# Kernel optimization log

Measured on AMD Instinct MI355X. Metric: run time of the kernel, lower is better.

Reference implementation:

```python
import jax, jax.numpy as jnp
import numpy as np

ALPHA = 4.0          # spikingjelly default surrogate.Sigmoid(alpha=4.0)
V_TH = 1.0           # IFNode default v_threshold
BN_EPS = 1e-5

@jax.custom_vjp
def spike(x):
    # heaviside forward
    return (x >= 0.0).astype(x.dtype)

def _spike_fwd(x):
    return spike(x), x

def _spike_bwd(x, g):
    s = jax.nn.sigmoid(ALPHA * x)
    return (g * ALPHA * s * (1.0 - s),)

spike.defvjp(_spike_fwd, _spike_bwd)

def if_node(x_seq):
    """Multi-step IF neuron: integrate, threshold, hard reset (v_reset=0),
    detach_reset=True. x_seq: [T, ...] -> spikes [T, ...]."""
    def step(v, xt):
        v = v + xt
        s = spike(v - V_TH)
        v = v * (1.0 - jax.lax.stop_gradient(s))  # detached hard reset to 0
        return v, s
    _, s_seq = jax.lax.scan(step, jnp.zeros_like(x_seq[0]), x_seq)
    return s_seq

def bn1d(x, gamma, beta):
    """Training-mode BatchNorm1d over flattened (T*B) batch dim. x: [T,B,F]."""
    m = x.mean(axis=(0, 1))
    v = x.var(axis=(0, 1))  # biased variance, matches torch normalization
    return (x - m) * jax.lax.rsqrt(v + BN_EPS) * gamma + beta

def setup_inputs() -> dict:
    key = jax.random.key(0)
    ks = jax.random.split(key, 12)
    T, B, C, H, W = 8, 64, 2, 128, 128
    F0, D, NC = C * H * W, 2048, 1000
    x = jax.random.uniform(ks[0], (T, B, C, H, W), dtype=jnp.float32)
    def kaiming(k, out_f, in_f):
        # kaiming_normal_ mode='fan_out', relu gain: std = sqrt(2/out_f)
        return jax.random.normal(k, (out_f, in_f), dtype=jnp.float32) * np.sqrt(2.0 / out_f)
    def bias(k, out_f, in_f):
        bound = 1.0 / np.sqrt(in_f)
        return jax.random.uniform(k, (out_f,), dtype=jnp.float32, minval=-bound, maxval=bound)
    inp = {"x": x}
    dims = [(D, F0), (D, D), (D, D)]
    for i, (o, f) in enumerate(dims):
        inp[f"W{i}"] = kaiming(ks[1 + i], o, f)
        inp[f"b{i}"] = bias(ks[4 + i], o, f)
        inp[f"g{i}"] = jnp.ones((o,), jnp.float32)
        inp[f"be{i}"] = jnp.zeros((o,), jnp.float32)
    inp["Wout"] = kaiming(ks[7], NC, D)
    inp["bout"] = bias(ks[8], NC, D)
    return inp

def reference(x, W0, b0, g0, be0, W1, b1, g1, be1, W2, b2, g2, be2, Wout, bout):
    T, B = x.shape[0], x.shape[1]
    h = x.reshape(T, B, -1)           # [T,B,32768]
    h = if_node(h)                    # sn0
    for Wl, bl, gl, bel in ((W0, b0, g0, be0), (W1, b1, g1, be1), (W2, b2, g2, be2)):
        h = jnp.einsum('tbi,oi->tbo', h, Wl) + bl
        h = bn1d(h, gl, bel)
        h = if_node(h)
    out = jnp.einsum('tbi,oi->tbo', h, Wout) + bout  # [T,B,1000]
    return out.mean(axis=0)           # [B,1000]
```

## Files before the change

### kernel.cpp

```cpp
#include <hip/hip_runtime.h>


#define T_STEPS 8
#define BATCH 64
#define F0 32768
#define DIM 2048
#define NROWS 512
#define NC 1000

typedef __attribute__((ext_vector_type(8))) short short8;
typedef __attribute__((ext_vector_type(4))) float f32x4;

__device__ __forceinline__ unsigned short bf16_rne(float f) {
    unsigned int u = __float_as_uint(f);
    u += 0x7FFFu + ((u >> 16) & 1u);
    return (unsigned short)(u >> 16);
}

#define BM 128
#define BN 128
#define BK 32

__global__ __launch_bounds__(256, 3) void gemm_splitk(
    const unsigned short* __restrict__ A, const float* __restrict__ W,
    float* __restrict__ part, int M, int N, int K, int Kpart, int Wrows)
{
    __shared__ unsigned short As[2][BM * BK];
    __shared__ unsigned short HL[2][BN * 64];

    const int gx = gridDim.x, gy = gridDim.y;
    const int nwg = gx * gy * gridDim.z;
    const int lid = blockIdx.x + gx * (blockIdx.y + gy * blockIdx.z);
    const int cpx = nwg >> 3;
    const int nid = (lid & 7) * cpx + (lid >> 3);
    const int bx  = nid % gx;
    const int by  = (nid / gx) % gy;
    const int kz  = nid / (gx * gy);

    const int tid  = threadIdx.x;
    const int lane = tid & 63;
    const int w    = tid >> 6;
    const int bm   = bx * BM;
    const int bn   = by * BN;
    const int ksteps = Kpart / BK;
    const int wm = (w >> 1) * 64;
    const int wn = (w & 1) * 64;
    const int kbase = kz * Kpart;

    const int a_sl  = ((lane & 3) ^ ((lane >> 3) & 3)) << 4;
    const int a_row = lane >> 2;

    const int wn_row = tid >> 3;
    const int wc4    = tid & 7;
    const int r7     = wn_row & 7;
    const int hi_off = (((wc4 >> 1) ^ r7) << 4) + (wc4 & 1) * 8;
    const int lo_off = ((((wc4 >> 1) + 4) ^ r7) << 4) + (wc4 & 1) * 8;

    const int l15 = lane & 15;
    const int a_ph = (((lane >> 4) ^ ((l15 >> 1) & 3)) << 4);
    const int h_ph = (((lane >> 4) ^ (lane & 7)) << 4);
    const int l_ph = ((((lane >> 4) + 4) ^ (lane & 7)) << 4);

    f32x4 acc[4][4] = {};
    float4 wv[4];

    auto issue_loads = [&](int buf, int kt) {
        const int k0 = kbase + kt * BK;
#pragma unroll
        for (int i = 0; i < 4; ++i) {
            const int rg = min(bn + wn_row + 32 * i, Wrows - 1);
            wv[i] = *(const float4*)&W[(size_t)rg * K + k0 + wc4 * 4];
        }
#pragma unroll
        for (int c = 0; c < 2; ++c) {
            const int row = w * 32 + c * 16 + a_row;
            const char* src = (const char*)A + ((size_t)(bm + row) * K + k0) * 2 + a_sl;
            __builtin_amdgcn_global_load_lds(
                (const __attribute__((address_space(1))) void*)src,
                (__attribute__((address_space(3))) void*)&As[buf][(w * 32 + c * 16) * BK],
                16, 0, 0);
        }
    };
    auto convert_write = [&](int buf) {
#pragma unroll
        for (int i = 0; i < 4; ++i) {
            const float vf[4] = {wv[i].x, wv[i].y, wv[i].z, wv[i].w};
            unsigned short h[4], l[4];
#pragma unroll
            for (int e = 0; e < 4; ++e) {
                h[e] = bf16_rne(vf[e]);
                l[e] = bf16_rne(vf[e] - __uint_as_float((unsigned int)h[e] << 16));
            }
            char* base = (char*)&HL[buf][0] + (wn_row + 32 * i) * 128;
            *(ushort4*)(base + hi_off) = make_ushort4(h[0], h[1], h[2], h[3]);
            *(ushort4*)(base + lo_off) = make_ushort4(l[0], l[1], l[2], l[3]);
        }
    };

    issue_loads(0, 0);
    convert_write(0);
    __syncthreads();

    int cur = 0;
    for (int kt = 0; kt < ksteps; ++kt) {
        const bool last = (kt + 1 == ksteps);
        if (!last) issue_loads(cur ^ 1, kt + 1);

        short8 a[4];
#pragma unroll
        for (int mi = 0; mi < 4; ++mi)
            a[mi] = *(const short8*)((const char*)&As[cur][0] + (wm + mi * 16 + l15) * 64 + a_ph);
#pragma unroll
        for (int ni = 0; ni < 4; ++ni) {
            const char* rp = (const char*)&HL[cur][0] + (wn + ni * 16 + l15) * 128;
            const short8 bh = *(const short8*)(rp + h_ph);
            const short8 bl = *(const short8*)(rp + l_ph);
#pragma unroll
            for (int mi = 0; mi < 4; ++mi) {
                acc[mi][ni] = __builtin_amdgcn_mfma_f32_16x16x32_bf16(a[mi], bh, acc[mi][ni], 0, 0, 0);
                acc[mi][ni] = __builtin_amdgcn_mfma_f32_16x16x32_bf16(a[mi], bl, acc[mi][ni], 0, 0, 0);
            }
        }
        if (!last) convert_write(cur ^ 1);
        __syncthreads();
        cur ^= 1;
    }

    const size_t zoff = (size_t)kz * M * N;
#pragma unroll
    for (int mi = 0; mi < 4; ++mi) {
        const int gr0 = bm + wm + mi * 16 + (lane >> 4) * 4;
#pragma unroll
        for (int ni = 0; ni < 4; ++ni) {
            const int gc = bn + wn + ni * 16 + (lane & 15);
            if (gc < N) {
#pragma unroll
                for (int e = 0; e < 4; ++e) {
                    const int gr = gr0 + e;
                    if (gr < M) part[zoff + (size_t)gr * N + gc] = acc[mi][ni][e];
                }
            }
        }
    }
}

__global__ __launch_bounds__(256) void reduce_bias(
    const float* __restrict__ part, const float* __restrict__ bias,
    float* __restrict__ out, int KS, int MN, int N)
{
    const int i4 = blockIdx.x * 256 + threadIdx.x;
    if (i4 * 4 >= MN) return;
    float4 s = make_float4(0.f, 0.f, 0.f, 0.f);
    for (int z = 0; z < KS; ++z) {
        const float4 p = *(const float4*)&part[(size_t)z * MN + i4 * 4];
        s.x += p.x; s.y += p.y; s.z += p.z; s.w += p.w;
    }
    const int col = (i4 * 4) % N;
    const float4 b = *(const float4*)&bias[col];
    s.x += b.x; s.y += b.y; s.z += b.z; s.w += b.w;
    *(float4*)&out[(size_t)i4 * 4] = s;
}

__global__ __launch_bounds__(256) void if0_kernel(
    const float* __restrict__ x, unsigned short* __restrict__ s)
{
    const size_t id4 = ((size_t)blockIdx.x * 256 + threadIdx.x) * 4;
    float v0 = 0.f, v1 = 0.f, v2 = 0.f, v3 = 0.f;
#pragma unroll
    for (int t = 0; t < T_STEPS; ++t) {
        const size_t idx = (size_t)t * (BATCH * (size_t)F0) + id4;
        const float4 xv = *(const float4*)&x[idx];
        ushort4 o;
        v0 += xv.x; if (v0 >= 1.f) { o.x = 0x3F80; v0 = 0.f; } else o.x = 0;
        v1 += xv.y; if (v1 >= 1.f) { o.y = 0x3F80; v1 = 0.f; } else o.y = 0;
        v2 += xv.z; if (v2 >= 1.f) { o.z = 0x3F80; v2 = 0.f; } else o.z = 0;
        v3 += xv.w; if (v3 >= 1.f) { o.w = 0x3F80; v3 = 0.f; } else o.w = 0;
        *(ushort4*)&s[idx] = o;
    }
}

__global__ __launch_bounds__(256) void bn_stats_if(
    const float* __restrict__ z, const float* __restrict__ g,
    const float* __restrict__ be, unsigned short* __restrict__ s)
{
    __shared__ float ssum[4][64], ssq[4][64];
    __shared__ float ssc[64], ssh[64];
    const int l = threadIdx.x & 63;
    const int q = threadIdx.x >> 6;
    const int f = blockIdx.x * 64 + l;
    float sum = 0.f, sq = 0.f;
    for (int r = q; r < NROWS; r += 4) {
        const float v = z[(size_t)r * DIM + f];
        sum += v; sq += v * v;
    }
    ssum[q][l] = sum; ssq[q][l] = sq;
    __syncthreads();
    if (threadIdx.x < 64) {
        float ts = 0.f, tq = 0.f;
#pragma unroll
        for (int i = 0; i < 4; ++i) { ts += ssum[i][l]; tq += ssq[i][l]; }
        const float mean = ts * (1.0f / NROWS);
        const float var  = tq * (1.0f / NROWS) - mean * mean;
        const float inv  = rsqrtf(var + 1e-5f);
        const float sc   = g[f] * inv;
        ssc[l] = sc;
        ssh[l] = be[f] - mean * sc;
    }
    __syncthreads();
    const float sc = ssc[l];
    const float sh = ssh[l];
    for (int b = q; b < BATCH; b += 4) {
        const int id = b * DIM + f;
        float v = 0.f;
#pragma unroll
        for (int t = 0; t < T_STEPS; ++t) {
            const size_t idx = (size_t)t * (BATCH * DIM) + id;
            v += z[idx] * sc + sh;
            if (v >= 1.0f) { s[idx] = 0x3F80; v = 0.f; }
            else           { s[idx] = 0; }
        }
    }
}

__global__ __launch_bounds__(256) void bn_stats_if_mean(
    const float* __restrict__ z, const float* __restrict__ g,
    const float* __restrict__ be, unsigned short* __restrict__ sbar)
{
    __shared__ float ssum[4][64], ssq[4][64];
    __shared__ float ssc[64], ssh[64];
    const int l = threadIdx.x & 63;
    const int q = threadIdx.x >> 6;
    const int f = blockIdx.x * 64 + l;
    float sum = 0.f, sq = 0.f;
    for (int r = q; r < NROWS; r += 4) {
        const float v = z[(size_t)r * DIM + f];
        sum += v; sq += v * v;
    }
    ssum[q][l] = sum; ssq[q][l] = sq;
    __syncthreads();
    if (threadIdx.x < 64) {
        float ts = 0.f, tq = 0.f;
#pragma unroll
        for (int i = 0; i < 4; ++i) { ts += ssum[i][l]; tq += ssq[i][l]; }
        const float mean = ts * (1.0f / NROWS);
        const float var  = tq * (1.0f / NROWS) - mean * mean;
        const float inv  = rsqrtf(var + 1e-5f);
        const float sc   = g[f] * inv;
        ssc[l] = sc;
        ssh[l] = be[f] - mean * sc;
    }
    __syncthreads();
    const float sc = ssc[l];
    const float sh = ssh[l];
    for (int b = q; b < BATCH; b += 4) {
        const int id = b * DIM + f;
        float v = 0.f;
        int cnt = 0;
#pragma unroll
        for (int t = 0; t < T_STEPS; ++t) {
            const size_t idx = (size_t)t * (BATCH * DIM) + id;
            v += z[idx] * sc + sh;
            if (v >= 1.0f) { cnt++; v = 0.f; }
        }
        sbar[id] = bf16_rne((float)cnt * 0.125f);
    }
}

extern "C" void kernel_launch(void* const* d_in, const int* in_sizes, int n_in,
                              void* d_out, int out_size, void* d_ws, size_t ws_size,
                              hipStream_t stream)
{
    const float* x    = (const float*)d_in[0];
    const float* W0   = (const float*)d_in[1];
    const float* b0   = (const float*)d_in[2];
    const float* g0   = (const float*)d_in[3];
    const float* be0  = (const float*)d_in[4];
    const float* W1   = (const float*)d_in[5];
    const float* b1   = (const float*)d_in[6];
    const float* g1   = (const float*)d_in[7];
    const float* be1  = (const float*)d_in[8];
    const float* W2   = (const float*)d_in[9];
    const float* b2   = (const float*)d_in[10];
    const float* g2   = (const float*)d_in[11];
    const float* be2  = (const float*)d_in[12];
    const float* Wout = (const float*)d_in[13];
    const float* bout = (const float*)d_in[14];
    float* out = (float*)d_out;
    (void)in_sizes; (void)n_in; (void)out_size; (void)ws_size;

    char* ws = (char*)d_ws;
    size_t off = 0;
    auto alloc = [&](size_t nbytes) {
        char* p = ws + off;
        off = (off + nbytes + 255) & ~(size_t)255;
        return p;
    };
    unsigned short* s0 = (unsigned short*)alloc((size_t)NROWS * F0 * 2);
    unsigned short* s1 = (unsigned short*)alloc((size_t)NROWS * DIM * 2);
    unsigned short* s2 = (unsigned short*)alloc((size_t)NROWS * DIM * 2);
    unsigned short* sb = (unsigned short*)alloc((size_t)128 * DIM * 2);
    float* z    = (float*)alloc((size_t)NROWS * DIM * 4);
    float* part = (float*)alloc((size_t)16 * NROWS * DIM * 4);

    const int MN = NROWS * DIM;

    if0_kernel<<<(BATCH * (size_t)F0) / 4 / 256, 256, 0, stream>>>(x, s0);

    gemm_splitk<<<dim3(NROWS / BM, DIM / BN, 16), 256, 0, stream>>>(
        s0, W0, part, NROWS, DIM, F0, F0 / 16, DIM);
    reduce_bias<<<MN / 4 / 256, 256, 0, stream>>>(part, b0, z, 16, MN, DIM);
    bn_stats_if<<<DIM / 64, 256, 0, stream>>>(z, g0, be0, s1);

    gemm_splitk<<<dim3(NROWS / BM, DIM / BN, 8), 256, 0, stream>>>(
        s1, W1, part, NROWS, DIM, DIM, DIM / 8, DIM);
    reduce_bias<<<MN / 4 / 256, 256, 0, stream>>>(part, b1, z, 8, MN, DIM);
    bn_stats_if<<<DIM / 64, 256, 0, stream>>>(z, g1, be1, s2);

    gemm_splitk<<<dim3(NROWS / BM, DIM / BN, 8), 256, 0, stream>>>(
        s2, W2, part, NROWS, DIM, DIM, DIM / 8, DIM);
    reduce_bias<<<MN / 4 / 256, 256, 0, stream>>>(part, b2, z, 8, MN, DIM);
    bn_stats_if_mean<<<DIM / 64, 256, 0, stream>>>(z, g2, be2, sb);

    gemm_splitk<<<dim3(1, (NC + BN - 1) / BN, 4), 256, 0, stream>>>(
        sb, Wout, part, BATCH, NC, DIM, DIM / 4, NC);
    reduce_bias<<<(BATCH * NC / 4 + 255) / 256, 256, 0, stream>>>(
        part, bout, out, 4, BATCH * NC, NC);
}
```

Measured before the change: 472.7 us.

## Restructure split-K GEMM to 512 threads with BK=64 single-buffered LDS

Rewrites the split-K GEMM kernel to use 8 waves per block (512 threads) with each wave computing a 64x32 sub-tile, and doubles the K step to 64. The LDS double buffering and the software prefetch of the next tile are removed: each iteration now loads, converts W to hi/lo bf16, syncs, computes and syncs again. The aim is more waves to hide latency and fewer loop iterations and barriers. In exchange, global-load latency is no longer overlapped with MFMA work inside a block, and the lower register budget from the wider launch bound may limit occupancy.

```diff
diff --git a/kernel.cpp b/kernel.cpp
--- a/kernel.cpp
+++ b/kernel.cpp
@@ -19,14 +19,20 @@
 
 #define BM 128
 #define BN 128
-#define BK 32
-
-__global__ __launch_bounds__(256, 3) void gemm_splitk(
+#define BK 64
+
+__device__ __forceinline__ short8 lds_frag(const unsigned short* base, int row, int kb) {
+    const int off = row * 128 + (kb ^ ((row & 7) << 4));
+    return *(const short8*)((const char*)base + off);
+}
+
+__global__ __launch_bounds__(512) void gemm_splitk(
     const unsigned short* __restrict__ A, const float* __restrict__ W,
     float* __restrict__ part, int M, int N, int K, int Kpart, int Wrows)
 {
-    __shared__ unsigned short As[2][BM * BK];
-    __shared__ unsigned short HL[2][BN * 64];
+    __shared__ unsigned short As[BM * BK];
+    __shared__ unsigned short Hs[BN * BK];
+    __shared__ unsigned short Ls[BN * BK];
 
     const int gx = gridDim.x, gy = gridDim.y;
     const int nwg = gx * gy * gridDim.z;
@@ -43,87 +49,78 @@
     const int bm   = bx * BM;
     const int bn   = by * BN;
     const int ksteps = Kpart / BK;
-    const int wm = (w >> 1) * 64;
-    const int wn = (w & 1) * 64;
-    const int kbase = kz * Kpart;
-
-    const int a_sl  = ((lane & 3) ^ ((lane >> 3) & 3)) << 4;
-    const int a_row = lane >> 2;
-
-    const int wn_row = tid >> 3;
-    const int wc4    = tid & 7;
-    const int r7     = wn_row & 7;
-    const int hi_off = (((wc4 >> 1) ^ r7) << 4) + (wc4 & 1) * 8;
-    const int lo_off = ((((wc4 >> 1) + 4) ^ r7) << 4) + (wc4 & 1) * 8;
-
-    const int l15 = lane & 15;
-    const int a_ph = (((lane >> 4) ^ ((l15 >> 1) & 3)) << 4);
-    const int h_ph = (((lane >> 4) ^ (lane & 7)) << 4);
-    const int l_ph = ((((lane >> 4) + 4) ^ (lane & 7)) << 4);
-
-    f32x4 acc[4][4] = {};
-    float4 wv[4];
-
-    auto issue_loads = [&](int buf, int kt) {
-        const int k0 = kbase + kt * BK;
-#pragma unroll
-        for (int i = 0; i < 4; ++i) {
-            const int rg = min(bn + wn_row + 32 * i, Wrows - 1);
-            wv[i] = *(const float4*)&W[(size_t)rg * K + k0 + wc4 * 4];
-        }
+    const int wm = (w >> 2) * 64;
+    const int wn = (w & 3) * 32;
+
+    f32x4 acc[4][2] = {};
+
+    for (int kt = 0; kt < ksteps; ++kt) {
+        const int k0 = kz * Kpart + kt * BK;
+
 #pragma unroll
         for (int c = 0; c < 2; ++c) {
-            const int row = w * 32 + c * 16 + a_row;
-            const char* src = (const char*)A + ((size_t)(bm + row) * K + k0) * 2 + a_sl;
+            const int r    = w * 16 + c * 8 + (lane >> 3);
+            const int colb = ((lane & 7) * 16) ^ ((r & 7) << 4);
+            const char* src = (const char*)A + ((size_t)(bm + r) * K + k0) * 2 + colb;
+            unsigned short* dst = &As[(w * 16 + c * 8) * BK];
             __builtin_amdgcn_global_load_lds(
                 (const __attribute__((address_space(1))) void*)src,
-                (__attribute__((address_space(3))) void*)&As[buf][(w * 32 + c * 16) * BK],
-                16, 0, 0);
-        }
-    };
-    auto convert_write = [&](int buf) {
+                (__attribute__((address_space(3))) void*)dst, 16, 0, 0);
+        }
+
+        float4 wv[4];
 #pragma unroll
         for (int i = 0; i < 4; ++i) {
+            const int q  = tid + 512 * i;
+            const int n  = q >> 4;
+            const int c4 = q & 15;
+            const int gn = min(bn + n, Wrows - 1);
+            wv[i] = *(const float4*)&W[(size_t)gn * K + k0 + c4 * 4];
+        }
+#pragma unroll
+        for (int i = 0; i < 4; ++i) {
+            const int q  = tid + 512 * i;
+            const int n  = q >> 4;
+            const int c4 = q & 15;
             const float vf[4] = {wv[i].x, wv[i].y, wv[i].z, wv[i].w};
             unsigned short h[4], l[4];
 #pragma unroll
             for (int e = 0; e < 4; ++e) {
                 h[e] = bf16_rne(vf[e]);
-                l[e] = bf16_rne(vf[e] - __uint_as_float((unsigned int)h[e] << 16));
+                const float hf = __uint_as_float((unsigned int)h[e] << 16);
+                l[e] = bf16_rne(vf[e] - hf);
             }
-            char* base = (char*)&HL[buf][0] + (wn_row + 32 * i) * 128;
-            *(ushort4*)(base + hi_off) = make_ushort4(h[0], h[1], h[2], h[3]);
-            *(ushort4*)(base + lo_off) = make_ushort4(l[0], l[1], l[2], l[3]);
-        }
-    };
-
-    issue_loads(0, 0);
-    convert_write(0);
-    __syncthreads();
-
-    int cur = 0;
-    for (int kt = 0; kt < ksteps; ++kt) {
-        const bool last = (kt + 1 == ksteps);
-        if (!last) issue_loads(cur ^ 1, kt + 1);
-
-        short8 a[4];
-#pragma unroll
-        for (int mi = 0; mi < 4; ++mi)
-            a[mi] = *(const short8*)((const char*)&As[cur][0] + (wm + mi * 16 + l15) * 64 + a_ph);
-#pragma unroll
-        for (int ni = 0; ni < 4; ++ni) {
-            const char* rp = (const char*)&HL[cur][0] + (wn + ni * 16 + l15) * 128;
-            const short8 bh = *(const short8*)(rp + h_ph);
-            const short8 bl = *(const short8*)(rp + l_ph);
-#pragma unroll
-            for (int mi = 0; mi < 4; ++mi) {
-                acc[mi][ni] = __builtin_amdgcn_mfma_f32_16x16x32_bf16(a[mi], bh, acc[mi][ni], 0, 0, 0);
-                acc[mi][ni] = __builtin_amdgcn_mfma_f32_16x16x32_bf16(a[mi], bl, acc[mi][ni], 0, 0, 0);
+            const int off = n * 128 + ((c4 * 8) ^ ((n & 7) << 4));
+            *(ushort4*)((char*)Hs + off) = make_ushort4(h[0], h[1], h[2], h[3]);
+            *(ushort4*)((char*)Ls + off) = make_ushort4(l[0], l[1], l[2], l[3]);
+        }
+
+        __syncthreads();
+
+#pragma unroll
+        for (int kk = 0; kk < 2; ++kk) {
+            const int kb = (kk * 32 + (lane >> 4) * 8) * 2;
+            short8 a[4], bh[2], bl[2];
+#pragma unroll
+            for (int i = 0; i < 4; ++i)
+                a[i] = lds_frag(As, wm + i * 16 + (lane & 15), kb);
+#pragma unroll
+            for (int i = 0; i < 2; ++i) {
+                const int r = wn + i * 16 + (lane & 15);
+                bh[i] = lds_frag(Hs, r, kb);
+                bl[i] = lds_frag(Ls, r, kb);
             }
-        }
-        if (!last) convert_write(cur ^ 1);
+#pragma unroll
+            for (int mi = 0; mi < 4; ++mi)
+#pragma unroll
+                for (int ni = 0; ni < 2; ++ni) {
+                    acc[mi][ni] = __builtin_amdgcn_mfma_f32_16x16x32_bf16(
+                        a[mi], bh[ni], acc[mi][ni], 0, 0, 0);
+                    acc[mi][ni] = __builtin_amdgcn_mfma_f32_16x16x32_bf16(
+                        a[mi], bl[ni], acc[mi][ni], 0, 0, 0);
+                }
+        }
         __syncthreads();
-        cur ^= 1;
     }
 
     const size_t zoff = (size_t)kz * M * N;
@@ -131,7 +128,7 @@
     for (int mi = 0; mi < 4; ++mi) {
         const int gr0 = bm + wm + mi * 16 + (lane >> 4) * 4;
 #pragma unroll
-        for (int ni = 0; ni < 4; ++ni) {
+        for (int ni = 0; ni < 2; ++ni) {
             const int gc = bn + wn + ni * 16 + (lane & 15);
             if (gc < N) {
 #pragma unroll
@@ -306,22 +303,22 @@
 
     if0_kernel<<<(BATCH * (size_t)F0) / 4 / 256, 256, 0, stream>>>(x, s0);
 
-    gemm_splitk<<<dim3(NROWS / BM, DIM / BN, 16), 256, 0, stream>>>(
+    gemm_splitk<<<dim3(NROWS / BM, DIM / BN, 16), 512, 0, stream>>>(
         s0, W0, part, NROWS, DIM, F0, F0 / 16, DIM);
     reduce_bias<<<MN / 4 / 256, 256, 0, stream>>>(part, b0, z, 16, MN, DIM);
     bn_stats_if<<<DIM / 64, 256, 0, stream>>>(z, g0, be0, s1);
 
-    gemm_splitk<<<dim3(NROWS / BM, DIM / BN, 8), 256, 0, stream>>>(
+    gemm_splitk<<<dim3(NROWS / BM, DIM / BN, 8), 512, 0, stream>>>(
         s1, W1, part, NROWS, DIM, DIM, DIM / 8, DIM);
     reduce_bias<<<MN / 4 / 256, 256, 0, stream>>>(part, b1, z, 8, MN, DIM);
     bn_stats_if<<<DIM / 64, 256, 0, stream>>>(z, g1, be1, s2);
 
-    gemm_splitk<<<dim3(NROWS / BM, DIM / BN, 8), 256, 0, stream>>>(
+    gemm_splitk<<<dim3(NROWS / BM, DIM / BN, 8), 512, 0, stream>>>(
         s2, W2, part, NROWS, DIM, DIM, DIM / 8, DIM);
     reduce_bias<<<MN / 4 / 256, 256, 0, stream>>>(part, b2, z, 8, MN, DIM);
     bn_stats_if_mean<<<DIM / 64, 256, 0, stream>>>(z, g2, be2, sb);
 
-    gemm_splitk<<<dim3(1, (NC + BN - 1) / BN, 4), 256, 0, stream>>>(
+    gemm_splitk<<<dim3(1, (NC + BN - 1) / BN, 4), 512, 0, stream>>>(
         sb, Wout, part, BATCH, NC, DIM, DIM / 4, NC);
     reduce_bias<<<(BATCH * NC / 4 + 255) / 256, 256, 0, stream>>>(
         part, bout, out, 4, BATCH * NC, NC);
```

Measured after the change: 400.1 us. -15.4%, faster.
